# Optimization experiments

Hardware: AMD Instinct MI355X
Metric: run time of the kernel (lower is better)

## Reference

```python
import jax, jax.numpy as jnp
import numpy as np
import math

B, S, D, H, FF = 32, 577, 768, 12, 3072
Dh = D // H
EPS = 1e-5


def layer_norm(x, w, b):
    mu = jnp.mean(x, axis=-1, keepdims=True)
    var = jnp.mean(jnp.square(x - mu), axis=-1, keepdims=True)
    return (x - mu) * jax.lax.rsqrt(var + EPS) * w + b


def setup_inputs() -> dict:
    key = jax.random.key(0)
    ks = jax.random.split(key, 12)
    s = 0.02
    return {
        "x": jax.random.normal(ks[0], (B, S, D), dtype=jnp.float32),
        "ln1_w": jnp.ones((D,), jnp.float32),
        "ln1_b": jnp.zeros((D,), jnp.float32),
        # stacked per-head Q/K/V projections (head order matches torch concat order)
        "Wq": jax.random.normal(ks[1], (H, D, Dh), jnp.float32) * s,
        "bq": jnp.zeros((H, Dh), jnp.float32),
        "Wk": jax.random.normal(ks[2], (H, D, Dh), jnp.float32) * s,
        "bk": jnp.zeros((H, Dh), jnp.float32),
        "Wv": jax.random.normal(ks[3], (H, D, Dh), jnp.float32) * s,
        "bv": jnp.zeros((H, Dh), jnp.float32),
        "Wo": jax.random.normal(ks[4], (D, D), jnp.float32) * s,
        "bo": jnp.zeros((D,), jnp.float32),
        "ln2_w": jnp.ones((D,), jnp.float32),
        "ln2_b": jnp.zeros((D,), jnp.float32),
        "W1": jax.random.normal(ks[5], (D, FF), jnp.float32) * s,
        "b1": jnp.zeros((FF,), jnp.float32),
        "W2": jax.random.normal(ks[6], (FF, D), jnp.float32) * s,
        "b2": jnp.zeros((D,), jnp.float32),
    }


def reference(x, ln1_w, ln1_b, Wq, bq, Wk, bk, Wv, bv, Wo, bo, ln2_w, ln2_b, W1, b1, W2, b2):
    # pre-norm attention
    h = layer_norm(x, ln1_w, ln1_b)  # [B,S,D]
    q = jnp.einsum('bsd,hde->bhse', h, Wq) + bq[:, None, :]
    k = jnp.einsum('bsd,hde->bhse', h, Wk) + bk[:, None, :]
    v = jnp.einsum('bsd,hde->bhse', h, Wv) + bv[:, None, :]
    scores = jnp.einsum('bhse,bhte->bhst', q, k) / math.sqrt(Dh)
    probs = jax.nn.softmax(scores, axis=-1)
    ctx = jnp.einsum('bhst,bhte->bhse', probs, v)  # [B,H,S,Dh]
    ctx = ctx.transpose(0, 2, 1, 3).reshape(B, S, H * Dh)  # concat heads
    attn_out = ctx @ Wo + bo
    x = x + attn_out
    # pre-norm MLP (exact GELU, as nn.GELU default)
    h2 = layer_norm(x, ln2_w, ln2_b)
    mlp = jax.nn.gelu(h2 @ W1 + b1, approximate=False) @ W2 + b2
    return x + mlp
```

## Files before the change

### kernel.cpp

```cpp
#include <hip/hip_runtime.h>
#include <hip/hip_bf16.h>
#include <stdint.h>

#define B_ 32
#define S_ 577
#define D_ 768
#define H_ 12
#define FF_ 3072
#define MROWS (B_*S_)

typedef __attribute__((ext_vector_type(8))) short sh8;
typedef __attribute__((ext_vector_type(4))) float f32x4;
typedef __attribute__((ext_vector_type(4))) unsigned short us4;

static __device__ __forceinline__ unsigned short f2b(float f) {
  __hip_bfloat16 h = __float2bfloat16(f);
  return *reinterpret_cast<unsigned short*>(&h);
}
static __device__ __forceinline__ float b2f(unsigned short u) {
  __hip_bfloat16 h;
  *reinterpret_cast<unsigned short*>(&h) = u;
  return __bfloat162float(h);
}

static __device__ __forceinline__ float fast_gelu(float v) {
  const float z = fabsf(v) * 0.70710678118f;
  const float t = __builtin_amdgcn_rcpf(__builtin_fmaf(0.3275911f, z, 1.0f));
  float p = 1.061405429f;
  p = __builtin_fmaf(p, t, -1.453152027f);
  p = __builtin_fmaf(p, t,  1.421413741f);
  p = __builtin_fmaf(p, t, -0.284496736f);
  p = __builtin_fmaf(p, t,  0.254829592f);
  p = p * t;
  const float e = __expf(-z * z);
  const float erf_abs = __builtin_fmaf(-p, e, 1.0f);
  const float erf_v = copysignf(erf_abs, v);
  const float hv = 0.5f * v;
  return __builtin_fmaf(hv, erf_v, hv);
}

#define GLOAD_LDS16(gp, lp) \
  __builtin_amdgcn_global_load_lds((const __attribute__((address_space(1))) unsigned int*)(gp), \
                                   (__attribute__((address_space(3))) unsigned int*)(lp), 16, 0, 0)

__global__ __launch_bounds__(256) void packT64(
    const float* __restrict__ src, unsigned short* __restrict__ dst, int K, int N)
{
  __shared__ unsigned short t[64][65];
  const int tid = threadIdx.x;
  const int c = tid & 63, r4 = tid >> 6;
  const int kb = blockIdx.y * 64, nb = blockIdx.x * 64;
#pragma unroll
  for (int p = 0; p < 16; ++p) {
    const int ko = p * 4 + r4;
    t[c][ko] = f2b(src[(size_t)(kb + ko) * N + nb + c]);
  }
  __syncthreads();
#pragma unroll
  for (int p = 0; p < 16; ++p) {
    const int rr = p * 4 + r4;
    dst[(size_t)(nb + rr) * K + kb + c] = t[rr][c];
  }
}

__global__ __launch_bounds__(256) void packQKV64(
    const float* __restrict__ Wq, const float* __restrict__ Wk, const float* __restrict__ Wv,
    unsigned short* __restrict__ dst)
{
  __shared__ unsigned short t[64][65];
  const int tid = threadIdx.x;
  const int c = tid & 63, r4 = tid >> 6;
  const int kb = blockIdx.x * 64;
  const int h = blockIdx.y;
  const int which = blockIdx.z;
  const float* src = ((which == 0) ? Wq : (which == 1) ? Wk : Wv) + (size_t)h * 768 * 64;
  const float scl = (which == 0) ? 0.125f : 1.0f;
#pragma unroll
  for (int p = 0; p < 16; ++p) {
    const int ko = p * 4 + r4;
    t[c][ko] = f2b(src[(size_t)(kb + ko) * 64 + c] * scl);
  }
  __syncthreads();
  unsigned short* db = dst + (size_t)(which * 768 + h * 64) * 768;
#pragma unroll
  for (int p = 0; p < 16; ++p) {
    const int rr = p * 4 + r4;
    db[(size_t)rr * 768 + kb + c] = t[rr][c];
  }
}

__global__ __launch_bounds__(256) void bias_pack(
    const float* __restrict__ bq, const float* __restrict__ bk, const float* __restrict__ bv,
    float* __restrict__ biasq)
{
  const int idx = blockIdx.x * 256 + threadIdx.x;
  if (idx < 2304) {
    const int wb = idx / 768, rb = idx - wb * 768;
    const float* bb = (wb == 0) ? bq : (wb == 1) ? bk : bv;
    biasq[idx] = bb[rb] * (wb == 0 ? 0.125f : 1.0f);
  }
}

__global__ __launch_bounds__(256) void ln_bf16(
    const float* __restrict__ x, const float* __restrict__ w, const float* __restrict__ bse,
    unsigned short* __restrict__ out)
{
  const int row = blockIdx.x;
  const int tid = threadIdx.x;
  const float* xr = x + (size_t)row * 768;
  float v0 = xr[tid], v1 = xr[tid + 256], v2 = xr[tid + 512];
  float s = v0 + v1 + v2;
  float ss = v0 * v0 + v1 * v1 + v2 * v2;
#pragma unroll
  for (int off = 32; off >= 1; off >>= 1) {
    s  += __shfl_xor(s, off);
    ss += __shfl_xor(ss, off);
  }
  __shared__ float red[8];
  const int wv = tid >> 6, ln = tid & 63;
  if (ln == 0) { red[wv] = s; red[wv + 4] = ss; }
  __syncthreads();
  s  = red[0] + red[1] + red[2] + red[3];
  ss = red[4] + red[5] + red[6] + red[7];
  const float mu = s * (1.f / 768.f);
  const float var = ss * (1.f / 768.f) - mu * mu;
  const float rs = rsqrtf(var + 1e-5f);
  unsigned short* orow = out + (size_t)row * 768;
  orow[tid]       = f2b((v0 - mu) * rs * w[tid]       + bse[tid]);
  orow[tid + 256] = f2b((v1 - mu) * rs * w[tid + 256] + bse[tid + 256]);
  orow[tid + 512] = f2b((v2 - mu) * rs * w[tid + 512] + bse[tid + 512]);
}

template<int EPI>
__global__ __launch_bounds__(256, 3) void gemm128(
    const unsigned short* __restrict__ A, const unsigned short* __restrict__ Bt,
    const float* __restrict__ bias, const float* __restrict__ res,
    unsigned short* __restrict__ obf, float* __restrict__ of32,
    int M, int N, int K)
{
  __shared__ __align__(16) unsigned short sAB[2][128 * 64];
  const int tid = threadIdx.x;
  const int wid = tid >> 6, ln = tid & 63;
  const int wr = wid >> 1, wc = wid & 1;
  const int l15 = ln & 15, lg = ln >> 4;
  const int l7 = l15 & 7;
  const int uo0 = ((lg) ^ l7) * 8;
  const int uo1 = ((4 + lg) ^ l7) * 8;
  const int srow = ln >> 3;
  const int scol = ((ln & 7) ^ srow) * 8;
  const int NT = K >> 6;

  const int gx = N >> 7;
  const int nwg = gridDim.x;
  const int q = nwg >> 3, r = nwg & 7;
  const int x = blockIdx.x & 7, ii = blockIdx.x >> 3;
  const int wg = (x < r ? x * (q + 1) : r * (q + 1) + (x - r) * q) + ii;
  const int bm = wg / gx, bn = wg - bm * gx;

  const int arow = wr * 64 + l15;
  const int brow = wc * 64 + l15;

  const unsigned short* ap0; const unsigned short* ap1;
  const unsigned short* ap2; const unsigned short* ap3;
  const unsigned short* bp0; const unsigned short* bp1;
  const unsigned short* bp2; const unsigned short* bp3;
  {
    int g0 = bm * 128 + (wid * 4 + 0) * 8 + srow; if (g0 >= M) g0 = M - 1;
    int g1 = bm * 128 + (wid * 4 + 1) * 8 + srow; if (g1 >= M) g1 = M - 1;
    int g2 = bm * 128 + (wid * 4 + 2) * 8 + srow; if (g2 >= M) g2 = M - 1;
    int g3 = bm * 128 + (wid * 4 + 3) * 8 + srow; if (g3 >= M) g3 = M - 1;
    ap0 = A + (size_t)g0 * K + scol; ap1 = A + (size_t)g1 * K + scol;
    ap2 = A + (size_t)g2 * K + scol; ap3 = A + (size_t)g3 * K + scol;
    const int b0 = bn * 128 + (wid * 4 + 0) * 8 + srow;
    bp0 = Bt + (size_t)b0 * K + scol;
    bp1 = bp0 + (size_t)8 * K; bp2 = bp0 + (size_t)16 * K; bp3 = bp0 + (size_t)24 * K;
  }
  unsigned short* const lA = sAB[0] + wid * 4 * 512;
  unsigned short* const lB = sAB[1] + wid * 4 * 512;

  f32x4 acc[4][4] = {};

  for (int t = 0; t < NT; ++t) {
    __syncthreads();
    GLOAD_LDS16(ap0, lA);        GLOAD_LDS16(ap1, lA + 512);
    GLOAD_LDS16(ap2, lA + 1024); GLOAD_LDS16(ap3, lA + 1536);
    GLOAD_LDS16(bp0, lB);        GLOAD_LDS16(bp1, lB + 512);
    GLOAD_LDS16(bp2, lB + 1024); GLOAD_LDS16(bp3, lB + 1536);
    ap0 += 64; ap1 += 64; ap2 += 64; ap3 += 64;
    bp0 += 64; bp1 += 64; bp2 += 64; bp3 += 64;
    asm volatile("s_waitcnt vmcnt(0)" ::: "memory");
    __syncthreads();

#pragma unroll
    for (int kk = 0; kk < 2; ++kk) {
      const int uo = kk ? uo1 : uo0;
      sh8 af[4], bf[4];
#pragma unroll
      for (int mi = 0; mi < 4; ++mi)
        af[mi] = *(const sh8*)(sAB[0] + (arow + mi * 16) * 64 + uo);
#pragma unroll
      for (int ni = 0; ni < 4; ++ni)
        bf[ni] = *(const sh8*)(sAB[1] + (brow + ni * 16) * 64 + uo);
#pragma unroll
      for (int mi = 0; mi < 4; ++mi)
#pragma unroll
        for (int ni = 0; ni < 4; ++ni)
          acc[mi][ni] = __builtin_amdgcn_mfma_f32_16x16x32_bf16(af[mi], bf[ni], acc[mi][ni], 0, 0, 0);
    }
  }

  constexpr int ESTR = 132;
  float* eps = (float*)sAB;
  const int ecol = (tid & 31) * 4;
  const int gcol = bn * 128 + ecol;
  const f32x4 bvh = *(const f32x4*)(bias + gcol);
  const int erow0 = tid >> 5;
#pragma unroll
  for (int pass = 0; pass < 4; ++pass) {
    __syncthreads();
    if (wr == (pass >> 1)) {
      const int mib = (pass & 1) * 2;
#pragma unroll
      for (int ml = 0; ml < 2; ++ml)
#pragma unroll
        for (int ni = 0; ni < 4; ++ni)
#pragma unroll
          for (int rr = 0; rr < 4; ++rr)
            eps[(ml * 16 + lg * 4 + rr) * ESTR + wc * 64 + ni * 16 + l15] = acc[mib + ml][ni][rr];
    }
    __syncthreads();
#pragma unroll
    for (int pp = 0; pp < 4; ++pp) {
      const int rl = pp * 8 + erow0;
      const int grow = bm * 128 + pass * 32 + rl;
      if (grow < M) {
        f32x4 v = *(const f32x4*)(eps + rl * ESTR + ecol);
        v += bvh;
        if (EPI == 2) {
#pragma unroll
          for (int e = 0; e < 4; ++e) v[e] = fast_gelu(v[e]);
        }
        if (EPI == 1) {
          const f32x4 rv = *(const f32x4*)(res + (size_t)grow * N + gcol);
          v += rv;
          *(f32x4*)(of32 + (size_t)grow * N + gcol) = v;
        } else {
          us4 o = { f2b(v[0]), f2b(v[1]), f2b(v[2]), f2b(v[3]) };
          *(us4*)(obf + (size_t)grow * N + gcol) = o;
        }
      }
    }
  }
}

__global__ __launch_bounds__(512) void attn(
    const unsigned short* __restrict__ qkv, unsigned short* __restrict__ ctx)
{
  constexpr int KP = 72;
  __shared__ __align__(16) unsigned short sQ[128 * KP];
  __shared__ __align__(16) unsigned short sK[64 * KP];
  __shared__ __align__(16) unsigned short sVT[64 * KP];
  __shared__ __align__(16) unsigned short sP[8][16 * KP];
  const int tid = threadIdx.x, wv = tid >> 6, ln = tid & 63;
  const int l15 = ln & 15, lg = ln >> 4;
  const int b = blockIdx.z, h = blockIdx.y, qt = blockIdx.x;
  const size_t base = (size_t)b * S_ * 2304 + h * 64;
  const unsigned short* qp = qkv + base;
  const unsigned short* kp = qkv + base + 768;
  const unsigned short* vp = qkv + base + 1536;

  {
    const int r = tid >> 2, c = (tid & 3) * 16;
    int row = qt * 128 + r; if (row >= S_) row = S_ - 1;
    const unsigned short* g = qp + (size_t)row * 2304 + c;
    *(sh8*)(sQ + r * KP + c)     = *(const sh8*)g;
    *(sh8*)(sQ + r * KP + c + 8) = *(const sh8*)(g + 8);
  }

  const int kr = tid >> 3, kc = (tid & 7) * 8;
  const unsigned short* krow = kp + (size_t)kr * 2304 + kc;
  unsigned short* const sKdst = sK + kr * KP + kc;
  const int ve = tid & 63, vkvb = tid >> 6;
  const unsigned short* vrow = vp + (size_t)vkvb * 8 * 2304 + ve;
  unsigned short* const sVdst = sVT + ve * KP + vkvb * 8;

  f32x4 oacc[4] = {};
  float m_run = -1e30f, l_run = 0.f;
  const int nt = (S_ + 63) / 64;
  for (int t = 0; t < nt; ++t) {
    __syncthreads();
    if (t < nt - 1) {
      *(sh8*)sKdst = *(const sh8*)krow;
      krow += (size_t)64 * 2304;
      {
        unsigned short val[8];
#pragma unroll
        for (int j = 0; j < 8; ++j) val[j] = vrow[(size_t)j * 2304];
        *(sh8*)sVdst = *(sh8*)val;
        vrow += (size_t)64 * 2304;
      }
    } else {
      {
        int row = t * 64 + kr; if (row >= S_) row = S_ - 1;
        *(sh8*)sKdst = *(const sh8*)(kp + (size_t)row * 2304 + kc);
      }
      {
        unsigned short val[8];
#pragma unroll
        for (int j = 0; j < 8; ++j) {
          int row = t * 64 + vkvb * 8 + j; if (row >= S_) row = S_ - 1;
          val[j] = vp[(size_t)row * 2304 + ve];
        }
        *(sh8*)sVdst = *(sh8*)val;
      }
    }
    __syncthreads();

    f32x4 sacc[4] = {};
#pragma unroll
    for (int kk = 0; kk < 2; ++kk) {
      sh8 bq = *(const sh8*)(sQ + (wv * 16 + l15) * KP + kk * 32 + lg * 8);
#pragma unroll
      for (int f = 0; f < 4; ++f) {
        sh8 ak = *(const sh8*)(sK + (f * 16 + l15) * KP + kk * 32 + lg * 8);
        sacc[f] = __builtin_amdgcn_mfma_f32_16x16x32_bf16(ak, bq, sacc[f], 0, 0, 0);
      }
    }

    if (t == nt - 1) {
#pragma unroll
      for (int f = 0; f < 4; ++f)
#pragma unroll
        for (int r = 0; r < 4; ++r)
          if (t * 64 + f * 16 + lg * 4 + r >= S_) sacc[f][r] = -1e30f;
    }
    float pmax = -1e30f;
#pragma unroll
    for (int f = 0; f < 4; ++f)
#pragma unroll
      for (int r = 0; r < 4; ++r) pmax = fmaxf(pmax, sacc[f][r]);
    pmax = fmaxf(pmax, __shfl_xor(pmax, 16));
    pmax = fmaxf(pmax, __shfl_xor(pmax, 32));
    const float mnew = fmaxf(m_run, pmax);
    const float alpha = __expf(m_run - mnew);
    float psum = 0.f;
    unsigned short pb[4][4];
#pragma unroll
    for (int f = 0; f < 4; ++f)
#pragma unroll
      for (int r = 0; r < 4; ++r) {
        const float p = __expf(sacc[f][r] - mnew);
        psum += p;
        pb[f][r] = f2b(p);
      }
    psum += __shfl_xor(psum, 16);
    psum += __shfl_xor(psum, 32);
    l_run = l_run * alpha + psum;
    m_run = mnew;
#pragma unroll
    for (int f = 0; f < 4; ++f) {
      oacc[f][0] *= alpha; oacc[f][1] *= alpha;
      oacc[f][2] *= alpha; oacc[f][3] *= alpha;
    }
#pragma unroll
    for (int f = 0; f < 4; ++f) {
      us4 pk = { pb[f][0], pb[f][1], pb[f][2], pb[f][3] };
      *(us4*)(sP[wv] + l15 * KP + f * 16 + lg * 4) = pk;
    }
    __syncthreads();

#pragma unroll
    for (int kk = 0; kk < 2; ++kk) {
      sh8 bp = *(const sh8*)(sP[wv] + l15 * KP + kk * 32 + lg * 8);
#pragma unroll
      for (int fe = 0; fe < 4; ++fe) {
        sh8 av = *(const sh8*)(sVT + (fe * 16 + l15) * KP + kk * 32 + lg * 8);
        oacc[fe] = __builtin_amdgcn_mfma_f32_16x16x32_bf16(av, bp, oacc[fe], 0, 0, 0);
      }
    }
  }

  const int qa = qt * 128 + wv * 16 + l15;
  if (qa < S_) {
    const float inv = 1.f / l_run;
    const size_t orow = ((size_t)b * S_ + qa) * 768 + h * 64;
#pragma unroll
    for (int fe = 0; fe < 4; ++fe) {
      unsigned short pk[4];
#pragma unroll
      for (int r = 0; r < 4; ++r) pk[r] = f2b(oacc[fe][r] * inv);
      *(us4*)(ctx + orow + fe * 16 + lg * 4) = *(us4*)pk;
    }
  }
}

extern "C" void kernel_launch(void* const* d_in, const int* in_sizes, int n_in,
                              void* d_out, int out_size, void* d_ws, size_t ws_size,
                              hipStream_t stream)
{
  const float* x    = (const float*)d_in[0];
  const float* ln1w = (const float*)d_in[1];
  const float* ln1b = (const float*)d_in[2];
  const float* Wq   = (const float*)d_in[3];
  const float* bq   = (const float*)d_in[4];
  const float* Wk   = (const float*)d_in[5];
  const float* bk   = (const float*)d_in[6];
  const float* Wv   = (const float*)d_in[7];
  const float* bv   = (const float*)d_in[8];
  const float* Wo   = (const float*)d_in[9];
  const float* bo   = (const float*)d_in[10];
  const float* ln2w = (const float*)d_in[11];
  const float* ln2b = (const float*)d_in[12];
  const float* W1   = (const float*)d_in[13];
  const float* b1   = (const float*)d_in[14];
  const float* W2   = (const float*)d_in[15];
  const float* b2   = (const float*)d_in[16];
  float* out = (float*)d_out;
  char* ws = (char*)d_ws;

  unsigned short* wqkvT = (unsigned short*)(ws + 0);
  unsigned short* woT   = (unsigned short*)(ws + 3538944);
  unsigned short* w1T   = (unsigned short*)(ws + 4718592);
  unsigned short* w2T   = (unsigned short*)(ws + 9437184);
  float*          biasq = (float*)(ws + 14155776);
  unsigned short* hbf   = (unsigned short*)(ws + 14164992);
  unsigned short* qkvb  = (unsigned short*)(ws + 42525696);
  unsigned short* ctxb  = (unsigned short*)(ws + 127607808);
  unsigned short* mlp1  = qkvb;

  packQKV64<<<dim3(12, 12, 3), 256, 0, stream>>>(Wq, Wk, Wv, wqkvT);
  bias_pack<<<9, 256, 0, stream>>>(bq, bk, bv, biasq);
  packT64<<<dim3(12, 12), 256, 0, stream>>>(Wo, woT, 768, 768);
  packT64<<<dim3(48, 12), 256, 0, stream>>>(W1, w1T, 768, 3072);
  packT64<<<dim3(12, 48), 256, 0, stream>>>(W2, w2T, 3072, 768);

  ln_bf16<<<MROWS, 256, 0, stream>>>(x, ln1w, ln1b, hbf);
  gemm128<0><<<145 * 18, 256, 0, stream>>>(hbf, wqkvT, biasq, nullptr, qkvb, nullptr,
                                           MROWS, 2304, 768);
  attn<<<dim3(5, 12, 32), 512, 0, stream>>>(qkvb, ctxb);
  gemm128<1><<<145 * 6, 256, 0, stream>>>(ctxb, woT, bo, x, nullptr, out,
                                          MROWS, 768, 768);
  ln_bf16<<<MROWS, 256, 0, stream>>>(out, ln2w, ln2b, hbf);
  gemm128<2><<<145 * 24, 256, 0, stream>>>(hbf, w1T, b1, nullptr, mlp1, nullptr,
                                           MROWS, 3072, 768);
  gemm128<1><<<145 * 6, 256, 0, stream>>>(mlp1, w2T, b2, out, nullptr, out,
                                          MROWS, 768, 3072);
}
```

Before: 473.9 us.

## Use two waves per GEMM block with 128x64 per-wave tiles

The 128x128 GEMM block now runs 128 threads (2 waves) instead of 256 (4 waves). Each wave computes a 128x64 sub-tile with 8x4 MFMA accumulators instead of 64x64, and loads 8 rows each of A and B into LDS. This doubles per-wave register reuse of the B fragments and halves the number of waves in each block, cutting LDS fragment reads relative to MFMA work. The cost is more accumulator registers and fewer waves per CU to hide global-load and LDS latency, with launch bounds changed to (128,4).

```diff
diff --git a/kernel.cpp b/kernel.cpp
--- a/kernel.cpp
+++ b/kernel.cpp
@@ -132,7 +132,7 @@
 }
 
 template<int EPI>
-__global__ __launch_bounds__(256, 3) void gemm128(
+__global__ __launch_bounds__(128, 4) void gemm128(
     const unsigned short* __restrict__ A, const unsigned short* __restrict__ Bt,
     const float* __restrict__ bias, const float* __restrict__ res,
     unsigned short* __restrict__ obf, float* __restrict__ of32,
@@ -141,7 +141,7 @@
   __shared__ __align__(16) unsigned short sAB[2][128 * 64];
   const int tid = threadIdx.x;
   const int wid = tid >> 6, ln = tid & 63;
-  const int wr = wid >> 1, wc = wid & 1;
+  const int wc = wid;
   const int l15 = ln & 15, lg = ln >> 4;
   const int l7 = l15 & 7;
   const int uo0 = ((lg) ^ l7) * 8;
@@ -157,55 +157,46 @@
   const int wg = (x < r ? x * (q + 1) : r * (q + 1) + (x - r) * q) + ii;
   const int bm = wg / gx, bn = wg - bm * gx;
 
-  const int arow = wr * 64 + l15;
   const int brow = wc * 64 + l15;
 
-  const unsigned short* ap0; const unsigned short* ap1;
-  const unsigned short* ap2; const unsigned short* ap3;
-  const unsigned short* bp0; const unsigned short* bp1;
-  const unsigned short* bp2; const unsigned short* bp3;
-  {
-    int g0 = bm * 128 + (wid * 4 + 0) * 8 + srow; if (g0 >= M) g0 = M - 1;
-    int g1 = bm * 128 + (wid * 4 + 1) * 8 + srow; if (g1 >= M) g1 = M - 1;
-    int g2 = bm * 128 + (wid * 4 + 2) * 8 + srow; if (g2 >= M) g2 = M - 1;
-    int g3 = bm * 128 + (wid * 4 + 3) * 8 + srow; if (g3 >= M) g3 = M - 1;
-    ap0 = A + (size_t)g0 * K + scol; ap1 = A + (size_t)g1 * K + scol;
-    ap2 = A + (size_t)g2 * K + scol; ap3 = A + (size_t)g3 * K + scol;
-    const int b0 = bn * 128 + (wid * 4 + 0) * 8 + srow;
-    bp0 = Bt + (size_t)b0 * K + scol;
-    bp1 = bp0 + (size_t)8 * K; bp2 = bp0 + (size_t)16 * K; bp3 = bp0 + (size_t)24 * K;
-  }
-  unsigned short* const lA = sAB[0] + wid * 4 * 512;
-  unsigned short* const lB = sAB[1] + wid * 4 * 512;
-
-  f32x4 acc[4][4] = {};
+  const unsigned short* ap[8];
+  const unsigned short* bp[8];
+#pragma unroll
+  for (int j = 0; j < 8; ++j) {
+    const int g = wid * 8 + j;
+    int ga = bm * 128 + g * 8 + srow; if (ga >= M) ga = M - 1;
+    ap[j] = A + (size_t)ga * K + scol;
+    const int gb = bn * 128 + g * 8 + srow;
+    bp[j] = Bt + (size_t)gb * K + scol;
+  }
+  unsigned short* const lA = sAB[0] + (wid * 8) * 512;
+  unsigned short* const lB = sAB[1] + (wid * 8) * 512;
+
+  f32x4 acc[8][4] = {};
 
   for (int t = 0; t < NT; ++t) {
     __syncthreads();
-    GLOAD_LDS16(ap0, lA);        GLOAD_LDS16(ap1, lA + 512);
-    GLOAD_LDS16(ap2, lA + 1024); GLOAD_LDS16(ap3, lA + 1536);
-    GLOAD_LDS16(bp0, lB);        GLOAD_LDS16(bp1, lB + 512);
-    GLOAD_LDS16(bp2, lB + 1024); GLOAD_LDS16(bp3, lB + 1536);
-    ap0 += 64; ap1 += 64; ap2 += 64; ap3 += 64;
-    bp0 += 64; bp1 += 64; bp2 += 64; bp3 += 64;
+#pragma unroll
+    for (int j = 0; j < 8; ++j) { GLOAD_LDS16(ap[j], lA + j * 512); ap[j] += 64; }
+#pragma unroll
+    for (int j = 0; j < 8; ++j) { GLOAD_LDS16(bp[j], lB + j * 512); bp[j] += 64; }
     asm volatile("s_waitcnt vmcnt(0)" ::: "memory");
     __syncthreads();
 
 #pragma unroll
     for (int kk = 0; kk < 2; ++kk) {
       const int uo = kk ? uo1 : uo0;
-      sh8 af[4], bf[4];
-#pragma unroll
-      for (int mi = 0; mi < 4; ++mi)
-        af[mi] = *(const sh8*)(sAB[0] + (arow + mi * 16) * 64 + uo);
+      sh8 bf[4];
 #pragma unroll
       for (int ni = 0; ni < 4; ++ni)
         bf[ni] = *(const sh8*)(sAB[1] + (brow + ni * 16) * 64 + uo);
 #pragma unroll
-      for (int mi = 0; mi < 4; ++mi)
+      for (int mi = 0; mi < 8; ++mi) {
+        const sh8 af = *(const sh8*)(sAB[0] + (l15 + mi * 16) * 64 + uo);
 #pragma unroll
         for (int ni = 0; ni < 4; ++ni)
-          acc[mi][ni] = __builtin_amdgcn_mfma_f32_16x16x32_bf16(af[mi], bf[ni], acc[mi][ni], 0, 0, 0);
+          acc[mi][ni] = __builtin_amdgcn_mfma_f32_16x16x32_bf16(af, bf[ni], acc[mi][ni], 0, 0, 0);
+      }
     }
   }
 
@@ -218,8 +209,8 @@
 #pragma unroll
   for (int pass = 0; pass < 4; ++pass) {
     __syncthreads();
-    if (wr == (pass >> 1)) {
-      const int mib = (pass & 1) * 2;
+    {
+      const int mib = pass * 2;
 #pragma unroll
       for (int ml = 0; ml < 2; ++ml)
 #pragma unroll
@@ -230,8 +221,8 @@
     }
     __syncthreads();
 #pragma unroll
-    for (int pp = 0; pp < 4; ++pp) {
-      const int rl = pp * 8 + erow0;
+    for (int pp = 0; pp < 8; ++pp) {
+      const int rl = pp * 4 + erow0;
       const int grow = bm * 128 + pass * 32 + rl;
       if (grow < M) {
         f32x4 v = *(const f32x4*)(eps + rl * ESTR + ecol);
@@ -435,14 +426,14 @@
   packT64<<<dim3(12, 48), 256, 0, stream>>>(W2, w2T, 3072, 768);
 
   ln_bf16<<<MROWS, 256, 0, stream>>>(x, ln1w, ln1b, hbf);
-  gemm128<0><<<145 * 18, 256, 0, stream>>>(hbf, wqkvT, biasq, nullptr, qkvb, nullptr,
+  gemm128<0><<<145 * 18, 128, 0, stream>>>(hbf, wqkvT, biasq, nullptr, qkvb, nullptr,
                                            MROWS, 2304, 768);
   attn<<<dim3(5, 12, 32), 512, 0, stream>>>(qkvb, ctxb);
-  gemm128<1><<<145 * 6, 256, 0, stream>>>(ctxb, woT, bo, x, nullptr, out,
+  gemm128<1><<<145 * 6, 128, 0, stream>>>(ctxb, woT, bo, x, nullptr, out,
                                           MROWS, 768, 768);
   ln_bf16<<<MROWS, 256, 0, stream>>>(out, ln2w, ln2b, hbf);
-  gemm128<2><<<145 * 24, 256, 0, stream>>>(hbf, w1T, b1, nullptr, mlp1, nullptr,
+  gemm128<2><<<145 * 24, 128, 0, stream>>>(hbf, w1T, b1, nullptr, mlp1, nullptr,
                                            MROWS, 3072, 768);
-  gemm128<1><<<145 * 6, 256, 0, stream>>>(mlp1, w2T, b2, out, nullptr, out,
+  gemm128<1><<<145 * 6, 128, 0, stream>>>(mlp1, w2T, b2, out, nullptr, out,
                                           MROWS, 768, 3072);
 }
```

Result: slower. 757.9 us (+59.9%).
